# Performance work log

Measured on AMD Instinct MI355X. Metric: run time of the kernel, lower is better.

The kernel has to match this reference:

```python
import jax, jax.numpy as jnp
import numpy as np


def setup_inputs() -> dict:
    key = jax.random.key(0)
    k1, k2 = jax.random.split(key)
    G, T, H, E, C = 8, 4096, 1024, 32, 64
    token_inputs = jax.random.normal(k1, (G, T, H), dtype=jnp.float32)
    W = jax.random.normal(k2, (H, E), dtype=jnp.float32) * 0.02  # default_kernel_init stddev
    b = jnp.zeros((E,), dtype=jnp.float32)
    return {"token_inputs": token_inputs, "W": W, "b": b,
            "num_experts": E, "expert_capacity": C}


def reference(token_inputs, W, b, num_experts, expert_capacity):
    # RouterWeights: dense projection to expert logits, computed in fp32.
    x = token_inputs.astype(jnp.float32)                      # [G, T, H]
    router_logits = jnp.einsum('gth,he->gte', x, W) + b        # [G, T, E]
    router_probs = jax.nn.softmax(router_logits, axis=-1)      # [G, T, E]

    # Experts-choose masked routing: each expert picks its top-C tokens.
    probs_et = jnp.swapaxes(router_probs, 1, 2)                # [G, E, T]
    gate, idx = jax.lax.top_k(probs_et, expert_capacity)       # [G, E, C]

    T = token_inputs.shape[1]
    # one-hot over the token axis -> dispatch mask [G, T, E, C]
    dispatch = jax.nn.one_hot(idx, T, dtype=jnp.float32)       # [G, E, C, T]
    dispatch = jnp.transpose(dispatch, (0, 3, 1, 2))           # [G, T, E, C]
    combine = dispatch * gate[:, None, :, :]                   # [G, T, E, C]

    # Router z-loss on raw logits.
    G_, T_, _ = router_logits.shape
    log_z = jax.nn.logsumexp(router_logits, axis=-1)           # [G, T]
    z_loss = jnp.sum(jnp.square(log_z), dtype=jnp.float32) / (G_ * T_)
    return combine, dispatch, z_loss
```

## Files before the change

kernel.cpp:

```cpp
#include <hip/hip_runtime.h>
#include <math.h>

#define G 8
#define T 4096
#define H 1024
#define E 32
#define C 64
#define NTOK (G*T)
#define COMBINE_SZ ((size_t)G*T*E*C)
#define KC 64
#define TBLK 128

__global__ __launch_bounds__(256) void k_router(
    const float* __restrict__ x, const float* __restrict__ W,
    const float* __restrict__ bias, float* __restrict__ probs_t,
    float* __restrict__ z_out)
{
    __shared__ float xs[TBLK][68];
    __shared__ float ws2[KC][32];
    __shared__ float lt[TBLK][33];

    const int tid  = threadIdx.x;
    const int lane = tid & 63;
    const int wv   = __builtin_amdgcn_readfirstlane(tid >> 6);
    const int blk  = blockIdx.x;

    float acc0[8] = {0,0,0,0,0,0,0,0};
    float acc1[8] = {0,0,0,0,0,0,0,0};

    for (int ch = 0; ch < H / KC; ++ch) {
        const int h0 = ch * KC;

        {
            const float4* __restrict__ src = (const float4*)(W + (size_t)h0 * E);
            float4* __restrict__ dst = (float4*)ws2;
            dst[tid]       = src[tid];
            dst[tid + 256] = src[tid + 256];
        }
        #pragma unroll
        for (int k = 0; k < 8; ++k) {
            const int f   = k * 256 + tid;
            const int tok = f >> 4;
            const int h4  = f & 15;
            const float4 v = *(const float4*)(x + (size_t)(blk * TBLK + tok) * H + h0 + h4 * 4);
            *(float4*)(&xs[tok][h4 * 4]) = v;
        }
        __syncthreads();

        for (int hh = 0; hh < KC; hh += 4) {
            const float4 xa = *(const float4*)(&xs[lane][hh]);
            const float4 xb = *(const float4*)(&xs[64 + lane][hh]);
            #pragma unroll
            for (int j = 0; j < 4; ++j) {
                const float4 w0 = *(const float4*)(&ws2[hh + j][wv * 8]);
                const float4 w1 = *(const float4*)(&ws2[hh + j][wv * 8 + 4]);
                const float a_ = (j == 0) ? xa.x : (j == 1) ? xa.y : (j == 2) ? xa.z : xa.w;
                const float b_ = (j == 0) ? xb.x : (j == 1) ? xb.y : (j == 2) ? xb.z : xb.w;
                acc0[0] = fmaf(a_, w0.x, acc0[0]);  acc1[0] = fmaf(b_, w0.x, acc1[0]);
                acc0[1] = fmaf(a_, w0.y, acc0[1]);  acc1[1] = fmaf(b_, w0.y, acc1[1]);
                acc0[2] = fmaf(a_, w0.z, acc0[2]);  acc1[2] = fmaf(b_, w0.z, acc1[2]);
                acc0[3] = fmaf(a_, w0.w, acc0[3]);  acc1[3] = fmaf(b_, w0.w, acc1[3]);
                acc0[4] = fmaf(a_, w1.x, acc0[4]);  acc1[4] = fmaf(b_, w1.x, acc1[4]);
                acc0[5] = fmaf(a_, w1.y, acc0[5]);  acc1[5] = fmaf(b_, w1.y, acc1[5]);
                acc0[6] = fmaf(a_, w1.z, acc0[6]);  acc1[6] = fmaf(b_, w1.z, acc1[6]);
                acc0[7] = fmaf(a_, w1.w, acc0[7]);  acc1[7] = fmaf(b_, w1.w, acc1[7]);
            }
        }
        __syncthreads();
    }

    #pragma unroll
    for (int e = 0; e < 8; ++e) {
        const float be = bias[wv * 8 + e];
        lt[lane][wv * 8 + e]      = acc0[e] + be;
        lt[64 + lane][wv * 8 + e] = acc1[e] + be;
    }
    __syncthreads();

    if (tid < TBLK) {
        float v[E];
        float m = -1e30f;
        #pragma unroll
        for (int e = 0; e < E; ++e) { v[e] = lt[tid][e]; m = fmaxf(m, v[e]); }
        float s = 0.f;
        #pragma unroll
        for (int e = 0; e < E; ++e) { v[e] = expf(v[e] - m); s += v[e]; }
        const float inv = 1.f / s;
        #pragma unroll
        for (int e = 0; e < E; ++e) lt[tid][e] = v[e] * inv;
        const float lz = m + logf(s);
        float zsq = lz * lz;
        #pragma unroll
        for (int off = 32; off; off >>= 1) zsq += __shfl_down(zsq, off, 64);
        if ((tid & 63) == 0) atomicAdd(z_out, zsq * (1.0f / (float)NTOK));
    }
    __syncthreads();

    const int g  = blk >> 5;
    const int tb = (blk & 31) * TBLK;
    #pragma unroll
    for (int j = 0; j < 8; ++j) {
        const int e = wv * 8 + j;
        float* __restrict__ col = probs_t + ((size_t)(g * E + e)) * T + tb;
        col[lane]      = lt[lane][e];
        col[64 + lane] = lt[64 + lane][e];
    }
}

__global__ __launch_bounds__(256) void k_topk(
    const float* __restrict__ probs_t, float* __restrict__ out)
{
    const int ge  = blockIdx.x;
    const int g   = ge >> 5;
    const int e   = ge & 31;
    const int tid = threadIdx.x;
    const float* __restrict__ col = probs_t + (size_t)ge * T;

    float vals[16];
    unsigned long long keys[16];
    #pragma unroll
    for (int j = 0; j < 16; ++j) {
        const int t = j * 256 + tid;
        const float p = col[t];
        unsigned u = __float_as_uint(p);
        u = (u & 0x80000000u) ? ~u : (u | 0x80000000u);
        keys[j] = ((unsigned long long)u << 32) | (unsigned)(4095 - t);
        vals[j] = p;
    }

    __shared__ unsigned long long wmax[4];
    __shared__ unsigned long long gk;

    for (int c = 0; c < C; ++c) {
        unsigned long long kmax = 0ull;
        #pragma unroll
        for (int j = 0; j < 16; ++j) kmax = (keys[j] > kmax) ? keys[j] : kmax;
        #pragma unroll
        for (int off = 32; off; off >>= 1) {
            const unsigned long long o = __shfl_xor(kmax, off, 64);
            kmax = (o > kmax) ? o : kmax;
        }
        if ((tid & 63) == 0) wmax[tid >> 6] = kmax;
        __syncthreads();
        if (tid == 0) {
            unsigned long long m = wmax[0];
            #pragma unroll
            for (int w = 1; w < 4; ++w) m = (wmax[w] > m) ? wmax[w] : m;
            gk = m;
        }
        __syncthreads();
        const unsigned long long gkey = gk;
        #pragma unroll
        for (int j = 0; j < 16; ++j) {
            if (keys[j] == gkey) {
                const int t = 4095 - (int)(gkey & 0xFFFFFFFFu);
                const size_t idx = ((((size_t)g * T + t) * E + e) * C + c);
                out[idx] = vals[j];
                out[idx + COMBINE_SZ] = 1.0f;
                keys[j] = 0ull;
            }
        }
    }
}

extern "C" void kernel_launch(void* const* d_in, const int* in_sizes, int n_in,
                              void* d_out, int out_size, void* d_ws, size_t ws_size,
                              hipStream_t stream) {
    const float* x = (const float*)d_in[0];
    const float* W = (const float*)d_in[1];
    const float* b = (const float*)d_in[2];
    float* out     = (float*)d_out;
    float* probs_t = (float*)d_ws;

    hipMemsetAsync(d_out, 0, (size_t)out_size * sizeof(float), stream);

    k_router<<<NTOK / TBLK, 256, 0, stream>>>(x, W, b, probs_t, out + 2 * COMBINE_SZ);
    k_topk<<<G * E, 256, 0, stream>>>(probs_t, out);
}
```

Measured before the change: 693.2 us.

## Double-buffer router GEMM tiles and rewrite top-k as single-wavefront grouped max

The router projection now prefetches the next x/W chunk into registers while computing on the current LDS buffer, then stores it into an alternate shared buffer. This is meant to overlap global loads with FMA work. The top-k kernel shrinks to one 64-lane wavefront per expert column, keeping cached per-group maxima in registers. Only the affected group is recomputed after each selection, which removes the block-wide barriers and shared-memory reductions. The cost is more register pressure (64 values plus prefetch registers) and doubled LDS in the router.

```diff
diff --git a/kernel.cpp b/kernel.cpp
--- a/kernel.cpp
+++ b/kernel.cpp
@@ -16,8 +16,8 @@
     const float* __restrict__ bias, float* __restrict__ probs_t,
     float* __restrict__ z_out)
 {
-    __shared__ float xs[TBLK][68];
-    __shared__ float ws2[KC][32];
+    __shared__ float xs[2][TBLK][68];
+    __shared__ float ws2[2][KC][32];
     __shared__ float lt[TBLK][33];
 
     const int tid  = threadIdx.x;
@@ -28,32 +28,59 @@
     float acc0[8] = {0,0,0,0,0,0,0,0};
     float acc1[8] = {0,0,0,0,0,0,0,0};
 
-    for (int ch = 0; ch < H / KC; ++ch) {
-        const int h0 = ch * KC;
-
-        {
-            const float4* __restrict__ src = (const float4*)(W + (size_t)h0 * E);
-            float4* __restrict__ dst = (float4*)ws2;
-            dst[tid]       = src[tid];
-            dst[tid + 256] = src[tid + 256];
-        }
+    float4 wr0, wr1;
+    float4 xr[8];
+
+    {
+        const float4* __restrict__ src = (const float4*)(W);
+        wr0 = src[tid];
+        wr1 = src[tid + 256];
         #pragma unroll
         for (int k = 0; k < 8; ++k) {
             const int f   = k * 256 + tid;
             const int tok = f >> 4;
             const int h4  = f & 15;
-            const float4 v = *(const float4*)(x + (size_t)(blk * TBLK + tok) * H + h0 + h4 * 4);
-            *(float4*)(&xs[tok][h4 * 4]) = v;
-        }
-        __syncthreads();
+            xr[k] = *(const float4*)(x + (size_t)(blk * TBLK + tok) * H + h4 * 4);
+        }
+    }
+    {
+        float4* __restrict__ dst = (float4*)ws2[0];
+        dst[tid]       = wr0;
+        dst[tid + 256] = wr1;
+        #pragma unroll
+        for (int k = 0; k < 8; ++k) {
+            const int f   = k * 256 + tid;
+            const int tok = f >> 4;
+            const int h4  = f & 15;
+            *(float4*)(&xs[0][tok][h4 * 4]) = xr[k];
+        }
+    }
+    __syncthreads();
+
+    for (int ch = 0; ch < H / KC; ++ch) {
+        const int b = ch & 1;
+
+        if (ch + 1 < H / KC) {
+            const int h0n = (ch + 1) * KC;
+            const float4* __restrict__ src = (const float4*)(W + (size_t)h0n * E);
+            wr0 = src[tid];
+            wr1 = src[tid + 256];
+            #pragma unroll
+            for (int k = 0; k < 8; ++k) {
+                const int f   = k * 256 + tid;
+                const int tok = f >> 4;
+                const int h4  = f & 15;
+                xr[k] = *(const float4*)(x + (size_t)(blk * TBLK + tok) * H + h0n + h4 * 4);
+            }
+        }
 
         for (int hh = 0; hh < KC; hh += 4) {
-            const float4 xa = *(const float4*)(&xs[lane][hh]);
-            const float4 xb = *(const float4*)(&xs[64 + lane][hh]);
+            const float4 xa = *(const float4*)(&xs[b][lane][hh]);
+            const float4 xb = *(const float4*)(&xs[b][64 + lane][hh]);
             #pragma unroll
             for (int j = 0; j < 4; ++j) {
-                const float4 w0 = *(const float4*)(&ws2[hh + j][wv * 8]);
-                const float4 w1 = *(const float4*)(&ws2[hh + j][wv * 8 + 4]);
+                const float4 w0 = *(const float4*)(&ws2[b][hh + j][wv * 8]);
+                const float4 w1 = *(const float4*)(&ws2[b][hh + j][wv * 8 + 4]);
                 const float a_ = (j == 0) ? xa.x : (j == 1) ? xa.y : (j == 2) ? xa.z : xa.w;
                 const float b_ = (j == 0) ? xb.x : (j == 1) ? xb.y : (j == 2) ? xb.z : xb.w;
                 acc0[0] = fmaf(a_, w0.x, acc0[0]);  acc1[0] = fmaf(b_, w0.x, acc1[0]);
@@ -67,6 +94,21 @@
             }
         }
         __syncthreads();
+
+        if (ch + 1 < H / KC) {
+            const int bn = b ^ 1;
+            float4* __restrict__ dst = (float4*)ws2[bn];
+            dst[tid]       = wr0;
+            dst[tid + 256] = wr1;
+            #pragma unroll
+            for (int k = 0; k < 8; ++k) {
+                const int f   = k * 256 + tid;
+                const int tok = f >> 4;
+                const int h4  = f & 15;
+                *(float4*)(&xs[bn][tok][h4 * 4]) = xr[k];
+            }
+            __syncthreads();
+        }
     }
 
     #pragma unroll
@@ -107,57 +149,86 @@
     }
 }
 
-__global__ __launch_bounds__(256) void k_topk(
+__global__ __launch_bounds__(64) void k_topk(
     const float* __restrict__ probs_t, float* __restrict__ out)
 {
-    const int ge  = blockIdx.x;
-    const int g   = ge >> 5;
-    const int e   = ge & 31;
-    const int tid = threadIdx.x;
+    const int ge   = blockIdx.x;
+    const int g    = ge >> 5;
+    const int e    = ge & 31;
+    const int lane = threadIdx.x;
     const float* __restrict__ col = probs_t + (size_t)ge * T;
 
-    float vals[16];
-    unsigned long long keys[16];
-    #pragma unroll
-    for (int j = 0; j < 16; ++j) {
-        const int t = j * 256 + tid;
-        const float p = col[t];
-        unsigned u = __float_as_uint(p);
-        u = (u & 0x80000000u) ? ~u : (u | 0x80000000u);
-        keys[j] = ((unsigned long long)u << 32) | (unsigned)(4095 - t);
-        vals[j] = p;
-    }
-
-    __shared__ unsigned long long wmax[4];
-    __shared__ unsigned long long gk;
+    unsigned v[64];
+    #pragma unroll
+    for (int j4 = 0; j4 < 16; ++j4) {
+        const float4 p = *(const float4*)(col + j4 * 256 + lane * 4);
+        {
+            unsigned u = __float_as_uint(p.x);
+            v[j4 * 4 + 0] = (u & 0x80000000u) ? ~u : (u | 0x80000000u);
+        }
+        {
+            unsigned u = __float_as_uint(p.y);
+            v[j4 * 4 + 1] = (u & 0x80000000u) ? ~u : (u | 0x80000000u);
+        }
+        {
+            unsigned u = __float_as_uint(p.z);
+            v[j4 * 4 + 2] = (u & 0x80000000u) ? ~u : (u | 0x80000000u);
+        }
+        {
+            unsigned u = __float_as_uint(p.w);
+            v[j4 * 4 + 3] = (u & 0x80000000u) ? ~u : (u | 0x80000000u);
+        }
+    }
+
+    unsigned long long gk[8];
+    #pragma unroll
+    for (int grp = 0; grp < 8; ++grp) {
+        unsigned long long m = 0ull;
+        #pragma unroll
+        for (int q = 0; q < 8; ++q) {
+            const int j = grp * 8 + q;
+            const int t = ((j >> 2) << 8) + lane * 4 + (j & 3);
+            const unsigned long long k =
+                ((unsigned long long)v[j] << 32) | (unsigned)(4095 - t);
+            m = (k > m) ? k : m;
+        }
+        gk[grp] = m;
+    }
 
     for (int c = 0; c < C; ++c) {
-        unsigned long long kmax = 0ull;
-        #pragma unroll
-        for (int j = 0; j < 16; ++j) kmax = (keys[j] > kmax) ? keys[j] : kmax;
+        unsigned long long best = gk[0];
+        #pragma unroll
+        for (int grp = 1; grp < 8; ++grp) best = (gk[grp] > best) ? gk[grp] : best;
         #pragma unroll
         for (int off = 32; off; off >>= 1) {
-            const unsigned long long o = __shfl_xor(kmax, off, 64);
-            kmax = (o > kmax) ? o : kmax;
-        }
-        if ((tid & 63) == 0) wmax[tid >> 6] = kmax;
-        __syncthreads();
-        if (tid == 0) {
-            unsigned long long m = wmax[0];
-            #pragma unroll
-            for (int w = 1; w < 4; ++w) m = (wmax[w] > m) ? wmax[w] : m;
-            gk = m;
-        }
-        __syncthreads();
-        const unsigned long long gkey = gk;
-        #pragma unroll
-        for (int j = 0; j < 16; ++j) {
-            if (keys[j] == gkey) {
-                const int t = 4095 - (int)(gkey & 0xFFFFFFFFu);
-                const size_t idx = ((((size_t)g * T + t) * E + e) * C + c);
-                out[idx] = vals[j];
-                out[idx + COMBINE_SZ] = 1.0f;
-                keys[j] = 0ull;
+            const unsigned long long o = __shfl_xor(best, off, 64);
+            best = (o > best) ? o : best;
+        }
+        const int t = 4095 - (int)(best & 0xFFFFFFFFu);
+        if (((t >> 2) & 63) == lane) {
+            const unsigned mu   = (unsigned)(best >> 32);
+            const unsigned orig = (mu & 0x80000000u) ? (mu & 0x7FFFFFFFu) : ~mu;
+            const size_t idx = ((((size_t)g * T + t) * E + e) * C + c);
+            out[idx] = __uint_as_float(orig);
+            out[idx + COMBINE_SZ] = 1.0f;
+            const int jw = ((t >> 8) << 2) | (t & 3);
+            const int gw = jw >> 3;
+            #pragma unroll
+            for (int grp = 0; grp < 8; ++grp) {
+                if (grp == gw) {
+                    unsigned long long m = 0ull;
+                    #pragma unroll
+                    for (int q = 0; q < 8; ++q) {
+                        const int j = grp * 8 + q;
+                        unsigned vv = v[j];
+                        if (j == jw) { vv = 0u; v[j] = 0u; }
+                        const int tq = ((j >> 2) << 8) + lane * 4 + (j & 3);
+                        const unsigned long long k =
+                            ((unsigned long long)vv << 32) | (unsigned)(4095 - tq);
+                        m = (k > m) ? k : m;
+                    }
+                    gk[grp] = m;
+                }
             }
         }
     }
@@ -175,5 +246,5 @@
     hipMemsetAsync(d_out, 0, (size_t)out_size * sizeof(float), stream);
 
     k_router<<<NTOK / TBLK, 256, 0, stream>>>(x, W, b, probs_t, out + 2 * COMBINE_SZ);
-    k_topk<<<G * E, 256, 0, stream>>>(probs_t, out);
+    k_topk<<<G * E, 64, 0, stream>>>(probs_t, out);
 }
```

Result: slower. 1.098 ms (+58.4%).

## Replace iterative top-k with threshold filter and rank-count selection

Applied to the files above, without the earlier changes.

The per-(group, expert) top-k drops the 64 serial rounds of block-wide argmax, each with two barriers. It now computes a threshold as the minimum over 64 four-lane group maxima, which guarantees at least C candidates above it. Survivors are compacted into shared memory with ballot and atomics, and each candidate's output slot comes from counting how many keys exceed it. The original probability is decoded from the key, so the separate value array goes away. The memset size is written as an explicit expression, and the kernel uses 32 KB of shared memory for the candidate list.

```diff
diff --git a/kernel.cpp b/kernel.cpp
--- a/kernel.cpp
+++ b/kernel.cpp
@@ -110,55 +110,84 @@
 __global__ __launch_bounds__(256) void k_topk(
     const float* __restrict__ probs_t, float* __restrict__ out)
 {
-    const int ge  = blockIdx.x;
-    const int g   = ge >> 5;
-    const int e   = ge & 31;
-    const int tid = threadIdx.x;
+    const int ge   = blockIdx.x;
+    const int g    = ge >> 5;
+    const int e    = ge & 31;
+    const int tid  = threadIdx.x;
+    const int lane = tid & 63;
+    const int wv   = tid >> 6;
     const float* __restrict__ col = probs_t + (size_t)ge * T;
 
-    float vals[16];
+    __shared__ unsigned long long sk[T];
+    __shared__ unsigned long long wmin[4];
+    __shared__ unsigned long long thr_s;
+    __shared__ int cnt;
+
+    if (tid == 0) cnt = 0;
+
     unsigned long long keys[16];
     #pragma unroll
     for (int j = 0; j < 16; ++j) {
         const int t = j * 256 + tid;
-        const float p = col[t];
-        unsigned u = __float_as_uint(p);
+        unsigned u = __float_as_uint(col[t]);
         u = (u & 0x80000000u) ? ~u : (u | 0x80000000u);
         keys[j] = ((unsigned long long)u << 32) | (unsigned)(4095 - t);
-        vals[j] = p;
-    }
-
-    __shared__ unsigned long long wmax[4];
-    __shared__ unsigned long long gk;
-
-    for (int c = 0; c < C; ++c) {
-        unsigned long long kmax = 0ull;
-        #pragma unroll
-        for (int j = 0; j < 16; ++j) kmax = (keys[j] > kmax) ? keys[j] : kmax;
-        #pragma unroll
-        for (int off = 32; off; off >>= 1) {
-            const unsigned long long o = __shfl_xor(kmax, off, 64);
-            kmax = (o > kmax) ? o : kmax;
-        }
-        if ((tid & 63) == 0) wmax[tid >> 6] = kmax;
-        __syncthreads();
-        if (tid == 0) {
-            unsigned long long m = wmax[0];
-            #pragma unroll
-            for (int w = 1; w < 4; ++w) m = (wmax[w] > m) ? wmax[w] : m;
-            gk = m;
-        }
-        __syncthreads();
-        const unsigned long long gkey = gk;
-        #pragma unroll
-        for (int j = 0; j < 16; ++j) {
-            if (keys[j] == gkey) {
-                const int t = 4095 - (int)(gkey & 0xFFFFFFFFu);
-                const size_t idx = ((((size_t)g * T + t) * E + e) * C + c);
-                out[idx] = vals[j];
-                out[idx + COMBINE_SZ] = 1.0f;
-                keys[j] = 0ull;
-            }
+    }
+
+    unsigned long long tm = keys[0];
+    #pragma unroll
+    for (int j = 1; j < 16; ++j) tm = (keys[j] > tm) ? keys[j] : tm;
+    unsigned long long gm = tm;
+    {
+        unsigned long long o = __shfl_xor(gm, 1, 64); gm = (o > gm) ? o : gm;
+        o = __shfl_xor(gm, 2, 64);                    gm = (o > gm) ? o : gm;
+    }
+    unsigned long long mn = gm;
+    #pragma unroll
+    for (int off = 4; off < 64; off <<= 1) {
+        const unsigned long long o = __shfl_xor(mn, off, 64);
+        mn = (o < mn) ? o : mn;
+    }
+    if (lane == 0) wmin[wv] = mn;
+    __syncthreads();
+    if (tid == 0) {
+        unsigned long long m = wmin[0];
+        #pragma unroll
+        for (int w = 1; w < 4; ++w) m = (wmin[w] < m) ? wmin[w] : m;
+        thr_s = m;
+    }
+    __syncthreads();
+    const unsigned long long thr = thr_s;
+
+    #pragma unroll
+    for (int j = 0; j < 16; ++j) {
+        const bool pred = (keys[j] >= thr);
+        const unsigned long long mask = __ballot(pred);
+        int base = 0;
+        if (lane == 0) {
+            const int nw = (int)__popcll(mask);
+            base = nw ? atomicAdd(&cnt, nw) : 0;
+        }
+        base = __shfl(base, 0, 64);
+        if (pred) {
+            const int pos = (int)__popcll(mask & ((1ull << lane) - 1ull));
+            sk[base + pos] = keys[j];
+        }
+    }
+    __syncthreads();
+    const int n = cnt;
+
+    for (int i = tid; i < n; i += 256) {
+        const unsigned long long k = sk[i];
+        int r = 0;
+        for (int j = 0; j < n; ++j) r += (sk[j] > k) ? 1 : 0;
+        if (r < C) {
+            const int t = 4095 - (int)(k & 0xFFFFFFFFu);
+            const unsigned mu   = (unsigned)(k >> 32);
+            const unsigned orig = (mu & 0x80000000u) ? (mu & 0x7FFFFFFFu) : ~mu;
+            const size_t idx = ((((size_t)g * T + t) * E + e) * C + r);
+            out[idx] = __uint_as_float(orig);
+            out[idx + COMBINE_SZ] = 1.0f;
         }
     }
 }
@@ -172,7 +201,7 @@
     float* out     = (float*)d_out;
     float* probs_t = (float*)d_ws;
 
-    hipMemsetAsync(d_out, 0, (size_t)out_size * sizeof(float), stream);
+    hipMemsetAsync(d_out, 0, (size_t)(2 * COMBINE_SZ + 1) * sizeof(float), stream);
 
     k_router<<<NTOK / TBLK, 256, 0, stream>>>(x, W, b, probs_t, out + 2 * COMBINE_SZ);
     k_topk<<<G * E, 256, 0, stream>>>(probs_t, out);
```

Result: no change. 685.7 us (-1.1%).
